# Optimization experiments

Hardware: AMD Instinct MI355X
Metric: run time of the kernel (lower is better)

The kernel has to match this reference:

```python
import jax, jax.numpy as jnp
import numpy as np


def segment_pool(labels, hidden):
    """Faithful vectorized version of get_entity_embedding_from_hidden_states.

    labels: [B, L] int (0=O, 1=B, 2=I); hidden: [B, L, H].
    Returns [B, L, H]: per-row, the first count_ones(row) slots hold the mean
    hidden state of each mention segment (segments delimited by label==1 over
    the nonzero-label token stream, flattened across the whole batch), rest 0.
    """
    B, L, H = hidden.shape
    N = B * L
    lab = labels.reshape(N)
    h = hidden.reshape(N, H)
    m = lab != 0
    # stable sort: nonzero-label tokens first, original order preserved
    perm = jnp.argsort(jnp.logical_not(m))
    lab_s = lab[perm]
    h_s = h[perm]
    m_s = m[perm]
    b = (lab_s == 1).astype(jnp.int32)
    cum = jnp.cumsum(b)                      # ones seen so far (nonzero stream)
    idx0 = jnp.argmax(b)                     # position of first B-tag (0 if none)
    p = jnp.arange(N)
    # chunk id of nonzero-stream token p: (#ones at positions <= p+idx0) - 1
    seg = cum[jnp.minimum(p + idx0, N - 1)] - 1
    valid = m_s & (seg >= 0)
    seg_ids = jnp.where(valid, seg, N)       # invalid tokens -> dumped segment N
    sums = jax.ops.segment_sum(h_s, seg_ids, num_segments=N + 1)[:N]
    counts = jax.ops.segment_sum(valid.astype(h.dtype), seg_ids, num_segments=N + 1)[:N]
    means = sums / jnp.maximum(counts, 1.0)[:, None]   # [N, H]
    # re-split per row: row b consumes count_ones(b) consecutive means, padded to L
    c = jnp.sum(labels == 1, axis=1)         # [B]
    starts = jnp.cumsum(c) - c               # exclusive prefix sum
    j = jnp.arange(L)
    gidx = jnp.clip(starts[:, None] + j[None, :], 0, N - 1)  # [B, L]
    out = means[gidx]                        # [B, L, H]
    return jnp.where((j[None, :] < c[:, None])[:, :, None], out, jnp.zeros((), hidden.dtype))


def setup_inputs() -> dict:
    key = jax.random.key(0)
    ks = jax.random.split(key, 8)
    B, L, H, E, P = 64, 512, 768, 1000, 300
    return {
        "bio_slot_labels": jax.random.randint(ks[0], (B, L), 0, 3, dtype=jnp.int32),
        "hidden_states": jax.random.normal(ks[1], (B, L, H), dtype=jnp.float32),
        "entity_type_embeddings": jax.random.normal(ks[2], (E, H), dtype=jnp.float32),
        "w1": jax.random.normal(ks[3], (H, H), dtype=jnp.float32) * 0.02,
        "b1": jnp.zeros((H,), dtype=jnp.float32),
        "w2": jax.random.normal(ks[4], (H, 3), dtype=jnp.float32) * 0.02,
        "b2": jnp.zeros((3,), dtype=jnp.float32),
        "w_mention": jax.random.normal(ks[5], (H, P), dtype=jnp.float32) * 0.02,
        "w_desc": jax.random.normal(ks[6], (H, P), dtype=jnp.float32) * 0.02,
    }


def reference(bio_slot_labels, hidden_states, entity_type_embeddings,
              w1, b1, w2, b2, w_mention, w_desc):
    # bio_mlp: Linear -> ReLU -> Linear -> LogSoftmax
    h1 = jax.nn.relu(jnp.einsum('blh,hk->blk', hidden_states, w1) + b1)
    bio_slot_logits = jax.nn.log_softmax(jnp.einsum('blh,hc->blc', h1, w2) + b2, axis=-1)
    predicted_bio_slot = jnp.argmax(bio_slot_logits, axis=-1)

    proj_desc = entity_type_embeddings @ w_desc          # [E, 300]

    def score(labels):
        pooled = segment_pool(labels, hidden_states)     # [B, L, H]
        proj_mention = jnp.einsum('blh,hp->blp', pooled, w_mention)
        dot = jnp.einsum('blp,ep->ble', proj_mention, proj_desc)
        return jax.nn.log_softmax(dot, axis=-1)

    return (bio_slot_logits, score(bio_slot_labels), score(predicted_bio_slot))
```

## Files before the change

### kernel.cpp

```cpp
#include <hip/hip_runtime.h>
#include <stdint.h>

__device__ inline float bf2f(unsigned short u) { return __uint_as_float(((unsigned int)u) << 16); }
__device__ inline unsigned short f2bf(float f) {
    unsigned int x = __float_as_uint(f);
    unsigned int r = x + 0x7fffu + ((x >> 16) & 1u);
    return (unsigned short)(r >> 16);
}

typedef __attribute__((ext_vector_type(8))) short bf16x8;
typedef __attribute__((ext_vector_type(4))) float f32x4;
typedef __attribute__((ext_vector_type(4))) int   v4i;
typedef __attribute__((ext_vector_type(4))) unsigned short u16x4;

#define FLAG_CAP 8192
#define MARGIN 0.02

__device__ inline void gload16(const void* g, void* l) {
    __builtin_amdgcn_global_load_lds(
        (const __attribute__((address_space(1))) void*)g,
        (__attribute__((address_space(3))) void*)l, 16, 0, 0);
}

__global__ __launch_bounds__(256) void gemm_bt(
    const unsigned short* __restrict__ A,
    const unsigned short* __restrict__ Bt,
    void* __restrict__ C,
    const int* __restrict__ Mdev,
    const int* __restrict__ rowMap,
    const float* __restrict__ fb1,
    const float* __restrict__ fw2,
    float* __restrict__ fpart,
    int M, int N, int K, int lda, int ldb, int ldc, int mode, int rowOff,
    size_t zA, int zMeta, int zMap, size_t zC)
{
    int zz = blockIdx.z;
    A += (size_t)zz * zA;
    if (Mdev) M = Mdev[zz * zMeta];
    if (rowMap) rowMap += (size_t)zz * zMap;

    int NT = gridDim.x;
    int p  = blockIdx.x + NT * blockIdx.y;
    int i8 = p >> 3;
    int mt = (p & 7) + 8 * (i8 / NT);
    int nt = i8 % NT;

    if (rowOff + mt * 128 >= M) return;

    __shared__ __align__(16) unsigned short As[128 * 64];
    __shared__ __align__(16) unsigned short Bs[128 * 64];

    int tid  = threadIdx.x;
    int lane = tid & 63, wave = tid >> 6;
    int wRow = (wave >> 1) * 64, wCol = (wave & 1) * 64;
    int mBase = mt * 128, nBase = nt * 128;
    int lm = lane & 15, kg = lane >> 4;
    int sr = tid >> 3;
    int sc = (tid & 7) * 8;

    f32x4 acc[4][4] = {};

    for (int k0 = 0; k0 < K; k0 += 64) {
        __syncthreads();
#pragma unroll
        for (int i = 0; i < 4; ++i) {
            int r = sr + 32 * i;
            int gm = rowOff + mBase + r; if (gm > M - 1) gm = M - 1;
            gload16(&A[(size_t)(gm - rowOff) * lda + k0 + sc], &As[wave * 512 + i * 2048]);
            int gn = nBase + r; if (gn > N - 1) gn = N - 1;
            gload16(&Bt[(size_t)gn * ldb + k0 + sc], &Bs[wave * 512 + i * 2048]);
        }
        __syncthreads();
#pragma unroll
        for (int ks = 0; ks < 2; ++ks) {
            bf16x8 af[4], bfr[4];
#pragma unroll
            for (int i = 0; i < 4; ++i) {
                af[i]  = *(const bf16x8*)&As[(wRow + i * 16 + lm) * 64 + ks * 32 + kg * 8];
                bfr[i] = *(const bf16x8*)&Bs[(wCol + i * 16 + lm) * 64 + ks * 32 + kg * 8];
            }
#pragma unroll
            for (int mi = 0; mi < 4; ++mi)
#pragma unroll
                for (int ni = 0; ni < 4; ++ni)
                    acc[mi][ni] = __builtin_amdgcn_mfma_f32_16x16x32_bf16(
                        af[mi], bfr[ni], acc[mi][ni], 0, 0, 0);
        }
    }

    int rbase = (lane >> 4) * 4;

    if (mode == 3) {
        float b1v[4], w2l[4][3];
#pragma unroll
        for (int ni = 0; ni < 4; ++ni) {
            int n = nBase + wCol + ni * 16 + lm;
            b1v[ni] = fb1[n];
#pragma unroll
            for (int c = 0; c < 3; ++c) w2l[ni][c] = fw2[n * 3 + c];
        }
#pragma unroll
        for (int mi = 0; mi < 4; ++mi) {
            float p2[4][3] = {};
#pragma unroll
            for (int ni = 0; ni < 4; ++ni)
#pragma unroll
                for (int r = 0; r < 4; ++r) {
                    float v = acc[mi][ni][r] + b1v[ni];
                    v = fmaxf(v, 0.f);
                    p2[r][0] += v * w2l[ni][0];
                    p2[r][1] += v * w2l[ni][1];
                    p2[r][2] += v * w2l[ni][2];
                }
#pragma unroll
            for (int r = 0; r < 4; ++r)
#pragma unroll
                for (int c = 0; c < 3; ++c) {
                    float s = p2[r][c];
                    s += __shfl_down(s, 8); s += __shfl_down(s, 4);
                    s += __shfl_down(s, 2); s += __shfl_down(s, 1);
                    p2[r][c] = s;
                }
            if (lm == 0) {
#pragma unroll
                for (int r = 0; r < 4; ++r) {
                    int row = mBase + wRow + mi * 16 + rbase + r;
#pragma unroll
                    for (int c = 0; c < 3; ++c)
                        atomicAdd(&fpart[(size_t)row * 3 + c], p2[r][c]);
                }
            }
        }
        return;
    }

#pragma unroll
    for (int mi = 0; mi < 4; ++mi) {
#pragma unroll
        for (int r = 0; r < 4; ++r) {
            int m = rowOff + mBase + wRow + mi * 16 + rbase + r;
            if (m >= M) continue;
            size_t crow = rowMap ? (size_t)rowMap[m] * ldc : (size_t)(m - rowOff) * ldc;
#pragma unroll
            for (int ni = 0; ni < 4; ++ni) {
                int n = nBase + wCol + ni * 16 + lm;
                if (n >= N) continue;
                float v = acc[mi][ni][r];
                if (mode == 2) ((float*)C)[(size_t)zz * zC + crow + n] = v;
                else           ((unsigned short*)C)[crow + n] = f2bf(v);
            }
        }
    }
}

__global__ __launch_bounds__(256) void prep_all(
    const float* __restrict__ ent, unsigned short* __restrict__ entB,
    const float* __restrict__ hidden, unsigned short* __restrict__ hiddenB,
    const float* __restrict__ wd, unsigned short* __restrict__ wdT,
    const float* __restrict__ w1, unsigned short* __restrict__ w1T,
    const float* __restrict__ wm, unsigned short* __restrict__ wmP,
    v4i* __restrict__ zreg)
{
    __shared__ float tile[32][33];
    int b = blockIdx.x, t = threadIdx.x;
    if (b < 373) {
        int i = b * 256 + t;
        if (i < 95312) { v4i z = {0, 0, 0, 0}; zreg[i] = z; }
        return;
    }
    b -= 373;
    if (b < 750) {
        int i = b * 256 + t;
        float4 v = ((const float4*)ent)[i];
        u16x4 o = { f2bf(v.x), f2bf(v.y), f2bf(v.z), f2bf(v.w) };
        ((u16x4*)entB)[i] = o;
        return;
    }
    b -= 750;
    if (b < 24576) {
        int i = b * 256 + t;
        float4 v = ((const float4*)hidden)[i];
        u16x4 o = { f2bf(v.x), f2bf(v.y), f2bf(v.z), f2bf(v.w) };
        ((u16x4*)hiddenB)[i] = o;
        return;
    }
    b -= 24576;
    if (b < 240 + 576) {
        const float* in; unsigned short* out; int R, C, bx, by;
        if (b < 240) { in = wd; out = wdT; R = 768; C = 300; bx = b % 10; by = b / 10; }
        else { int bb = b - 240; in = w1; out = w1T; R = 768; C = 768; bx = bb % 24; by = bb / 24; }
        int tx = t & 31, ty = t >> 5;
        int c0 = bx * 32, r0 = by * 32;
#pragma unroll
        for (int i = 0; i < 4; ++i) {
            int r = r0 + ty + i * 8, c = c0 + tx;
            if (r < R && c < C) tile[ty + i * 8][tx] = in[(size_t)r * C + c];
        }
        __syncthreads();
#pragma unroll
        for (int i = 0; i < 4; ++i) {
            int orow = c0 + ty + i * 8, ocol = r0 + tx;
            if (orow < C && ocol < R) out[(size_t)orow * R + ocol] = f2bf(tile[tx][ty + i * 8]);
        }
        return;
    }
    b -= 816;
    {
        int idx = b * 256 + t;
        if (idx < 768 * 300) wmP[(size_t)(idx / 300) * 320 + (idx % 300)] = f2bf(wm[idx]);
    }
}

__global__ void bio_final2(const float* __restrict__ part, const float* __restrict__ b2,
                           float* __restrict__ out0, int* __restrict__ predLab,
                           int* __restrict__ flagCnt, int* __restrict__ flagList)
{
    int t = blockIdx.x * 256 + threadIdx.x;
    double a[3];
#pragma unroll
    for (int c = 0; c < 3; ++c) a[c] = (double)part[(size_t)t * 3 + c] + (double)b2[c];
    double mx = a[0]; if (a[1] > mx) mx = a[1]; if (a[2] > mx) mx = a[2];
    double ls = mx + log(exp(a[0] - mx) + exp(a[1] - mx) + exp(a[2] - mx));
    out0[t * 3 + 0] = (float)(a[0] - ls);
    out0[t * 3 + 1] = (float)(a[1] - ls);
    out0[t * 3 + 2] = (float)(a[2] - ls);
    int pbest = 0; double bv = a[0];
    if (a[1] > bv) { bv = a[1]; pbest = 1; }
    if (a[2] > bv) { bv = a[2]; pbest = 2; }
    predLab[t] = pbest;
    double second = -1e300;
#pragma unroll
    for (int c = 0; c < 3; ++c) if (c != pbest && a[c] > second) second = a[c];
    if (bv - second < MARGIN) {
        int i = atomicAdd(flagCnt, 1);
        if (i < FLAG_CAP) flagList[i] = t;
    }
}

__global__ __launch_bounds__(256) void h1_bio_gemm(
    const float* __restrict__ hidden, const int* __restrict__ flagList,
    const float* __restrict__ W,
    const float* __restrict__ b1, const float* __restrict__ w2,
    float* __restrict__ part, const int* __restrict__ Mdev, int partStride)
{
    int M = *Mdev; if (M > FLAG_CAP) M = FLAG_CAP;
    if (M <= 0) return;
    int m0 = blockIdx.x * 64, n0 = blockIdx.y * 64;
    if (m0 >= M) return;
    __shared__ float AsT[16][64];
    __shared__ float Ws[16][64];
    int tx = threadIdx.x, ty = threadIdx.y;
    int tid = ty * 16 + tx;
    float acc[4][4] = {};

    for (int k0 = 0; k0 < 768; k0 += 16) {
        __syncthreads();
        {
            int row = tid >> 2, seg = (tid & 3) * 4;
            int gm = m0 + row; if (gm > M - 1) gm = M - 1;
            float4 v = *(const float4*)&hidden[(size_t)flagList[gm] * 768 + k0 + seg];
            AsT[seg + 0][row] = v.x; AsT[seg + 1][row] = v.y;
            AsT[seg + 2][row] = v.z; AsT[seg + 3][row] = v.w;
        }
        {
            int row = tid >> 4, seg = (tid & 15) * 4;
            *(float4*)&Ws[row][seg] = *(const float4*)&W[(size_t)(k0 + row) * 768 + n0 + seg];
        }
        __syncthreads();
#pragma unroll
        for (int kk = 0; kk < 16; ++kk) {
            float4 av = *(const float4*)&AsT[kk][ty * 4];
            float4 bv = *(const float4*)&Ws[kk][tx * 4];
            float a[4] = {av.x, av.y, av.z, av.w};
            float b[4] = {bv.x, bv.y, bv.z, bv.w};
#pragma unroll
            for (int i = 0; i < 4; ++i)
#pragma unroll
                for (int j = 0; j < 4; ++j)
                    acc[i][j] += a[i] * b[j];
        }
    }

    float b1v[4], w2l[4][3];
#pragma unroll
    for (int j = 0; j < 4; ++j) {
        int n = n0 + tx * 4 + j;
        b1v[j] = b1[n];
#pragma unroll
        for (int c = 0; c < 3; ++c) w2l[j][c] = w2[n * 3 + c];
    }
    float p[4][3] = {};
#pragma unroll
    for (int i = 0; i < 4; ++i)
#pragma unroll
        for (int j = 0; j < 4; ++j) {
            float v = acc[i][j] + b1v[j];
            v = fmaxf(v, 0.f);
#pragma unroll
            for (int c = 0; c < 3; ++c) p[i][c] += v * w2l[j][c];
        }
#pragma unroll
    for (int i = 0; i < 4; ++i)
#pragma unroll
        for (int c = 0; c < 3; ++c) {
            float s = p[i][c];
            s += __shfl_down(s, 8); s += __shfl_down(s, 4);
            s += __shfl_down(s, 2); s += __shfl_down(s, 1);
            p[i][c] = s;
        }
    if (tx == 0) {
#pragma unroll
        for (int i = 0; i < 4; ++i) {
            int t = m0 + ty * 4 + i;
            if (t >= M) continue;
#pragma unroll
            for (int c = 0; c < 3; ++c)
                part[(size_t)blockIdx.y * partStride + (size_t)t * 3 + c] = p[i][c];
        }
    }
}

__global__ __launch_bounds__(1024) void seg_prep2(
    const int* __restrict__ labels, int* predLab,
    int* __restrict__ streamTok, int* __restrict__ cumArr,
    int* __restrict__ meta, int* __restrict__ rowC, int* __restrict__ mapArr,
    int* __restrict__ segFirst,
    const float* __restrict__ partF, const float* __restrict__ b2,
    const int* __restrict__ flagList, const int* __restrict__ flagCnt, int partStride)
{
    int setz = blockIdx.x;
    int t = threadIdx.x;

    if (setz == 1) {
        int cnt = *flagCnt; if (cnt > FLAG_CAP) cnt = FLAG_CAP;
        for (int i = t; i < cnt; i += 1024) {
            double a[3] = {(double)b2[0], (double)b2[1], (double)b2[2]};
#pragma unroll
            for (int blk = 0; blk < 12; ++blk)
#pragma unroll
                for (int c = 0; c < 3; ++c)
                    a[c] += (double)partF[(size_t)blk * partStride + (size_t)i * 3 + c];
            int pbest = 0; double bv = a[0];
            if (a[1] > bv) { bv = a[1]; pbest = 1; }
            if (a[2] > bv) { bv = a[2]; pbest = 2; }
            predLab[flagList[i]] = pbest;
        }
        __syncthreads();
    }

    const int* lab = setz ? predLab : labels;
    int* sTok = streamTok + setz * 32768;
    int* sCum = cumArr + setz * 32768;
    int* mt   = meta + setz * 64;
    int* rC   = rowC + setz * 64;
    int* mp   = mapArr + setz * 32768;
    int* sf   = segFirst + setz * 32768;

    __shared__ int sM[1024], sB[1024];
    __shared__ int sRowC[64], sRowStart[64];
    __shared__ int sIdx0;
    if (t == 0) sIdx0 = 0x7fffffff;
    int base = t * 32;
    int vals[32];
#pragma unroll
    for (int j = 0; j < 8; ++j) {
        v4i v = ((const v4i*)lab)[t * 8 + j];
        vals[4 * j + 0] = v[0]; vals[4 * j + 1] = v[1];
        vals[4 * j + 2] = v[2]; vals[4 * j + 3] = v[3];
    }
    int mc = 0, bc = 0;
#pragma unroll
    for (int i = 0; i < 32; ++i) { mc += (vals[i] != 0); bc += (vals[i] == 1); }
    sM[t] = mc; sB[t] = bc; __syncthreads();
    for (int off = 1; off < 1024; off <<= 1) {
        int vm = 0, vb = 0;
        if (t >= off) { vm = sM[t - off]; vb = sB[t - off]; }
        __syncthreads();
        sM[t] += vm; sB[t] += vb;
        __syncthreads();
    }
    int mBase = sM[t] - mc, bBase = sB[t] - bc;
    int mRun = 0, bRun = 0;
#pragma unroll
    for (int i = 0; i < 32; ++i) {
        int v = vals[i];
        if (v != 0) {
            int q = mBase + mRun;
            sTok[q] = base + i;
            int isB = (v == 1);
            sCum[q] = bBase + bRun + isB;
            if (isB && (bBase + bRun) == 0) sIdx0 = q;
            mRun += 1; bRun += isB;
        }
    }
    if ((t & 15) == 0) sRowStart[t >> 4] = bBase;
    __syncthreads();
    if ((t & 15) == 0) {
        int b = t >> 4;
        sRowC[b] = sB[t + 15] - sRowStart[b];
        rC[b] = sRowC[b];
    }
    if (t == 1023) { mt[0] = sB[1023]; mt[1] = sM[1023]; }
    if (t == 0) mt[2] = (sIdx0 == 0x7fffffff) ? 0 : sIdx0;
    __syncthreads();
    for (int idx = t; idx < 32768; idx += 1024) {
        int b = idx >> 9, j = idx & 511;
        if (j < sRowC[b]) mp[sRowStart[b] + j] = idx;
    }

    int K = sM[1023], numB = sB[1023];
    int idx0 = (sIdx0 == 0x7fffffff) ? 0 : sIdx0;
    for (int q = t; q < K; q += 1024) {
        int qq = q + idx0;
        int c  = (qq < K) ? sCum[qq] : numB;
        int sg = c - 1;
        if (sg < 0) continue;
        int sp = -1;
        if (q > 0) {
            int qq2 = qq - 1;
            int c2  = (qq2 < K) ? sCum[qq2] : numB;
            sp = c2 - 1;
        }
        if (sg != sp) sf[sg] = q;
    }
}

__global__ __launch_bounds__(192) void seg_means2(
    const unsigned short* __restrict__ hiddenB, const int* __restrict__ streamTok,
    const int* __restrict__ segFirst, const int* __restrict__ meta,
    unsigned short* __restrict__ means, size_t zMeans)
{
    int setz = blockIdx.y;
    const int* mt = meta + setz * 64;
    int s = blockIdx.x;
    int numB = mt[0];
    if (s >= numB) return;
    const int* st = streamTok + setz * 32768;
    const int* sf = segFirst + setz * 32768;
    int q0 = sf[s];
    int q1 = (s + 1 < numB) ? sf[s + 1] : mt[1];
    int cnt = q1 - q0;
    int t = threadIdx.x;
    float a0 = 0.f, a1 = 0.f, a2 = 0.f, a3 = 0.f;
    for (int i = 0; i < cnt; ++i) {
        const unsigned short* hr = hiddenB + (size_t)st[q0 + i] * 768;
        u16x4 v = *(const u16x4*)&hr[t * 4];
        a0 += bf2f(v[0]); a1 += bf2f(v[1]); a2 += bf2f(v[2]); a3 += bf2f(v[3]);
    }
    float fc = (float)cnt;
    u16x4 o = { f2bf(a0 / fc), f2bf(a1 / fc), f2bf(a2 / fc), f2bf(a3 / fc) };
    *(u16x4*)&means[(size_t)setz * zMeans + (size_t)s * 768 + t * 4] = o;
}

__global__ __launch_bounds__(256) void softmax_rows2(float* __restrict__ outBase,
                                                     const int* __restrict__ rowCBase,
                                                     size_t zC)
{
    float* out = outBase + (size_t)blockIdx.y * zC;
    const int* rowC = rowCBase + blockIdx.y * 64;
    int v = blockIdx.x;
    int b = v >> 9, j = v & 511;
    int t = threadIdx.x;
    float* row = out + (size_t)v * 1000;
    if (j >= rowC[b]) {
        for (int e = t; e < 1000; e += 256) row[e] = -6.907755278982137f;
        return;
    }
    __shared__ float red[256];
    float x0 = row[t];
    float x1 = row[t + 256];
    float x2 = row[t + 512];
    bool has3 = (t + 768) < 1000;
    float x3 = has3 ? row[t + 768] : -1e30f;
    float mx = fmaxf(fmaxf(x0, x1), fmaxf(x2, x3));
    red[t] = mx; __syncthreads();
    for (int st = 128; st > 0; st >>= 1) { if (t < st) red[t] = fmaxf(red[t], red[t + st]); __syncthreads(); }
    float M = red[0]; __syncthreads();
    float sm = expf(x0 - M) + expf(x1 - M) + expf(x2 - M) + (has3 ? expf(x3 - M) : 0.f);
    red[t] = sm; __syncthreads();
    for (int st = 128; st > 0; st >>= 1) { if (t < st) red[t] += red[t + st]; __syncthreads(); }
    float ls = M + logf(red[0]);
    row[t]       = x0 - ls;
    row[t + 256] = x1 - ls;
    row[t + 512] = x2 - ls;
    if (has3) row[t + 768] = x3 - ls;
}

extern "C" void kernel_launch(void* const* d_in, const int* in_sizes, int n_in,
                              void* d_out, int out_size, void* d_ws, size_t ws_size,
                              hipStream_t stream)
{
    (void)in_sizes; (void)n_in; (void)out_size; (void)ws_size;
    const int*   labels = (const int*)d_in[0];
    const float* hidden = (const float*)d_in[1];
    const float* ent    = (const float*)d_in[2];
    const float* w1     = (const float*)d_in[3];
    const float* b1     = (const float*)d_in[4];
    const float* w2     = (const float*)d_in[5];
    const float* b2     = (const float*)d_in[6];
    const float* wm     = (const float*)d_in[7];
    const float* wd     = (const float*)d_in[8];

    char* ws = (char*)d_ws;
    size_t off = 0;
    auto alloc = [&](size_t bytes) {
        void* p = ws + off;
        off = (off + bytes + 255) & ~(size_t)255;
        return p;
    };
    int* meta      = (int*)alloc(512);
    int* rowC      = (int*)alloc(512);
    int* predLab   = (int*)alloc(32768 * 4);
    int* streamTok = (int*)alloc(2 * 32768 * 4);
    int* cumArr    = (int*)alloc(2 * 32768 * 4);
    int* segFirst  = (int*)alloc(2 * 32768 * 4);
    int* mapArr    = (int*)alloc(2 * 32768 * 4);
    int* flagList  = (int*)alloc(FLAG_CAP * 4);
    unsigned short* entB = (unsigned short*)alloc((size_t)1000 * 768 * 2);
    unsigned short* wdT  = (unsigned short*)alloc((size_t)300 * 768 * 2);
    unsigned short* W2t  = (unsigned short*)alloc((size_t)1000 * 768 * 2);
    unsigned short* w1T  = (unsigned short*)alloc((size_t)768 * 768 * 2);
    unsigned short* hiddenB = (unsigned short*)alloc((size_t)32768 * 768 * 2);
    float* partF = (float*)alloc((size_t)12 * FLAG_CAP * 3 * 4);
    char* zbase = (char*)alloc(1524992);
    unsigned short* pd  = (unsigned short*)zbase;
    unsigned short* wmP = (unsigned short*)(zbase + 640000);
    float* part         = (float*)(zbase + 1131520);
    int* flagCnt        = (int*)(zbase + 1524736);
    unsigned short* means = (unsigned short*)alloc((size_t)2 * 32768 * 768 * 2);

    float* out0 = (float*)d_out;
    float* out1 = out0 + 98304;

    prep_all<<<27415, 256, 0, stream>>>(ent, entB, hidden, hiddenB, wd, wdT,
                                        w1, w1T, wm, wmP, (v4i*)zbase);

    gemm_bt<<<dim3(3, 8), 256, 0, stream>>>(entB, wdT, pd, nullptr, nullptr,
                                            nullptr, nullptr, nullptr,
                                            1000, 300, 768, 768, 768, 320, 0, 0,
                                            0, 0, 0, 0);
    gemm_bt<<<dim3(6, 8), 256, 0, stream>>>(pd, wmP, W2t, nullptr, nullptr,
                                            nullptr, nullptr, nullptr,
                                            1000, 768, 320, 320, 320, 768, 0, 0,
                                            0, 0, 0, 0);

    gemm_bt<<<dim3(6, 256), 256, 0, stream>>>(hiddenB, w1T, nullptr, nullptr, nullptr,
                                              b1, w2, part,
                                              32768, 768, 768, 768, 768, 0, 3, 0,
                                              0, 0, 0, 0);
    bio_final2<<<128, 256, 0, stream>>>(part, b2, out0, predLab, flagCnt, flagList);
    h1_bio_gemm<<<dim3(FLAG_CAP / 64, 12), dim3(16, 16), 0, stream>>>(
        hidden, flagList, w1, b1, w2, partF, flagCnt, FLAG_CAP * 3);

    seg_prep2<<<2, 1024, 0, stream>>>(labels, predLab, streamTok, cumArr, meta, rowC,
                                      mapArr, segFirst, partF, b2, flagList, flagCnt,
                                      FLAG_CAP * 3);
    seg_means2<<<dim3(32768, 2), 192, 0, stream>>>(hiddenB, streamTok, segFirst, meta,
                                                   means, (size_t)32768 * 768);
    gemm_bt<<<dim3(8, 256, 2), 256, 0, stream>>>(means, W2t, out1, meta, mapArr,
                                                 nullptr, nullptr, nullptr,
                                                 0, 1000, 768, 768, 768, 1000, 2, 0,
                                                 (size_t)32768 * 768, 64, 32768,
                                                 (size_t)32768 * 1000);
    softmax_rows2<<<dim3(32768, 2), 256, 0, stream>>>(out1, rowC, (size_t)32768 * 1000);
}
```

Baseline: 807.7 us.

## Merge small GEMM launches into combined kernels and vectorize row softmax

The generic GEMM kernel becomes a device function, and the small entity-projection GEMMs are packed into the same launches as the big bio GEMM and the bio-final step. This removes several kernel launches and their tail idle time. The block swizzle now uses a plain mt/nt index, which changes the order tiles run in and may affect cache reuse. The row log-softmax now uses float4 loads and wave shuffle reductions in place of a shared-memory tree, cutting barriers and memory instructions on a large memory-bound pass.

```diff
diff --git a/kernel.cpp b/kernel.cpp
--- a/kernel.cpp
+++ b/kernel.cpp
@@ -22,7 +22,7 @@
         (__attribute__((address_space(3))) void*)l, 16, 0, 0);
 }
 
-__global__ __launch_bounds__(256) void gemm_bt(
+static __device__ inline void dev_gemm(
     const unsigned short* __restrict__ A,
     const unsigned short* __restrict__ Bt,
     void* __restrict__ C,
@@ -31,24 +31,12 @@
     const float* __restrict__ fb1,
     const float* __restrict__ fw2,
     float* __restrict__ fpart,
-    int M, int N, int K, int lda, int ldb, int ldc, int mode, int rowOff,
-    size_t zA, int zMeta, int zMap, size_t zC)
-{
-    int zz = blockIdx.z;
-    A += (size_t)zz * zA;
-    if (Mdev) M = Mdev[zz * zMeta];
-    if (rowMap) rowMap += (size_t)zz * zMap;
-
-    int NT = gridDim.x;
-    int p  = blockIdx.x + NT * blockIdx.y;
-    int i8 = p >> 3;
-    int mt = (p & 7) + 8 * (i8 / NT);
-    int nt = i8 % NT;
-
-    if (rowOff + mt * 128 >= M) return;
-
-    __shared__ __align__(16) unsigned short As[128 * 64];
-    __shared__ __align__(16) unsigned short Bs[128 * 64];
+    int M, int N, int K, int lda, int ldb, int ldc, int mode,
+    int mt, int nt,
+    unsigned short* As, unsigned short* Bs)
+{
+    if (Mdev) M = *Mdev;
+    if (mt * 128 >= M) return;
 
     int tid  = threadIdx.x;
     int lane = tid & 63, wave = tid >> 6;
@@ -65,8 +53,8 @@
 #pragma unroll
         for (int i = 0; i < 4; ++i) {
             int r = sr + 32 * i;
-            int gm = rowOff + mBase + r; if (gm > M - 1) gm = M - 1;
-            gload16(&A[(size_t)(gm - rowOff) * lda + k0 + sc], &As[wave * 512 + i * 2048]);
+            int gm = mBase + r; if (gm > M - 1) gm = M - 1;
+            gload16(&A[(size_t)gm * lda + k0 + sc], &As[wave * 512 + i * 2048]);
             int gn = nBase + r; if (gn > N - 1) gn = N - 1;
             gload16(&Bt[(size_t)gn * ldb + k0 + sc], &Bs[wave * 512 + i * 2048]);
         }
@@ -138,84 +126,26 @@
     for (int mi = 0; mi < 4; ++mi) {
 #pragma unroll
         for (int r = 0; r < 4; ++r) {
-            int m = rowOff + mBase + wRow + mi * 16 + rbase + r;
+            int m = mBase + wRow + mi * 16 + rbase + r;
             if (m >= M) continue;
-            size_t crow = rowMap ? (size_t)rowMap[m] * ldc : (size_t)(m - rowOff) * ldc;
+            size_t crow = rowMap ? (size_t)rowMap[m] * ldc : (size_t)m * ldc;
 #pragma unroll
             for (int ni = 0; ni < 4; ++ni) {
                 int n = nBase + wCol + ni * 16 + lm;
                 if (n >= N) continue;
                 float v = acc[mi][ni][r];
-                if (mode == 2) ((float*)C)[(size_t)zz * zC + crow + n] = v;
+                if (mode == 2) ((float*)C)[crow + n] = v;
                 else           ((unsigned short*)C)[crow + n] = f2bf(v);
             }
         }
     }
 }
 
-__global__ __launch_bounds__(256) void prep_all(
-    const float* __restrict__ ent, unsigned short* __restrict__ entB,
-    const float* __restrict__ hidden, unsigned short* __restrict__ hiddenB,
-    const float* __restrict__ wd, unsigned short* __restrict__ wdT,
-    const float* __restrict__ w1, unsigned short* __restrict__ w1T,
-    const float* __restrict__ wm, unsigned short* __restrict__ wmP,
-    v4i* __restrict__ zreg)
-{
-    __shared__ float tile[32][33];
-    int b = blockIdx.x, t = threadIdx.x;
-    if (b < 373) {
-        int i = b * 256 + t;
-        if (i < 95312) { v4i z = {0, 0, 0, 0}; zreg[i] = z; }
-        return;
-    }
-    b -= 373;
-    if (b < 750) {
-        int i = b * 256 + t;
-        float4 v = ((const float4*)ent)[i];
-        u16x4 o = { f2bf(v.x), f2bf(v.y), f2bf(v.z), f2bf(v.w) };
-        ((u16x4*)entB)[i] = o;
-        return;
-    }
-    b -= 750;
-    if (b < 24576) {
-        int i = b * 256 + t;
-        float4 v = ((const float4*)hidden)[i];
-        u16x4 o = { f2bf(v.x), f2bf(v.y), f2bf(v.z), f2bf(v.w) };
-        ((u16x4*)hiddenB)[i] = o;
-        return;
-    }
-    b -= 24576;
-    if (b < 240 + 576) {
-        const float* in; unsigned short* out; int R, C, bx, by;
-        if (b < 240) { in = wd; out = wdT; R = 768; C = 300; bx = b % 10; by = b / 10; }
-        else { int bb = b - 240; in = w1; out = w1T; R = 768; C = 768; bx = bb % 24; by = bb / 24; }
-        int tx = t & 31, ty = t >> 5;
-        int c0 = bx * 32, r0 = by * 32;
-#pragma unroll
-        for (int i = 0; i < 4; ++i) {
-            int r = r0 + ty + i * 8, c = c0 + tx;
-            if (r < R && c < C) tile[ty + i * 8][tx] = in[(size_t)r * C + c];
-        }
-        __syncthreads();
-#pragma unroll
-        for (int i = 0; i < 4; ++i) {
-            int orow = c0 + ty + i * 8, ocol = r0 + tx;
-            if (orow < C && ocol < R) out[(size_t)orow * R + ocol] = f2bf(tile[tx][ty + i * 8]);
-        }
-        return;
-    }
-    b -= 816;
-    {
-        int idx = b * 256 + t;
-        if (idx < 768 * 300) wmP[(size_t)(idx / 300) * 320 + (idx % 300)] = f2bf(wm[idx]);
-    }
-}
-
-__global__ void bio_final2(const float* __restrict__ part, const float* __restrict__ b2,
-                           float* __restrict__ out0, int* __restrict__ predLab,
-                           int* __restrict__ flagCnt, int* __restrict__ flagList)
-{
-    int t = blockIdx.x * 256 + threadIdx.x;
+static __device__ inline void dev_final2(int t, const float* __restrict__ part,
+                                         const float* __restrict__ b2,
+                                         float* __restrict__ out0, int* __restrict__ predLab,
+                                         int* __restrict__ flagCnt, int* __restrict__ flagList)
+{
     double a[3];
 #pragma unroll
     for (int c = 0; c < 3; ++c) a[c] = (double)part[(size_t)t * 3 + c] + (double)b2[c];
@@ -237,6 +167,116 @@
     }
 }
 
+__global__ __launch_bounds__(256) void k_gemms1(
+    const unsigned short* __restrict__ hiddenB, const unsigned short* __restrict__ w1T,
+    const float* __restrict__ b1, const float* __restrict__ w2, float* __restrict__ part,
+    const unsigned short* __restrict__ entB, const unsigned short* __restrict__ wdT,
+    unsigned short* __restrict__ pd)
+{
+    __shared__ __align__(16) unsigned short As[128 * 64];
+    __shared__ __align__(16) unsigned short Bs[128 * 64];
+    int bx = blockIdx.x;
+    if (bx < 1536) {
+        dev_gemm(hiddenB, w1T, nullptr, nullptr, nullptr, b1, w2, part,
+                 32768, 768, 768, 768, 768, 0, 3, bx / 6, bx % 6, As, Bs);
+    } else {
+        bx -= 1536;
+        dev_gemm(entB, wdT, pd, nullptr, nullptr, nullptr, nullptr, nullptr,
+                 1000, 300, 768, 768, 768, 320, 0, bx / 3, bx % 3, As, Bs);
+    }
+}
+
+__global__ __launch_bounds__(256) void k_gemms2(
+    const unsigned short* __restrict__ pd, const unsigned short* __restrict__ wmP,
+    unsigned short* __restrict__ W2t,
+    const float* __restrict__ part, const float* __restrict__ b2,
+    float* __restrict__ out0, int* __restrict__ predLab,
+    int* __restrict__ flagCnt, int* __restrict__ flagList)
+{
+    __shared__ __align__(16) unsigned short As[128 * 64];
+    __shared__ __align__(16) unsigned short Bs[128 * 64];
+    int bx = blockIdx.x;
+    if (bx < 48) {
+        dev_gemm(pd, wmP, W2t, nullptr, nullptr, nullptr, nullptr, nullptr,
+                 1000, 768, 320, 320, 320, 768, 0, bx / 6, bx % 6, As, Bs);
+    } else {
+        dev_final2((bx - 48) * 256 + threadIdx.x, part, b2, out0, predLab,
+                   flagCnt, flagList);
+    }
+}
+
+__global__ __launch_bounds__(256) void gemm_score(
+    const unsigned short* __restrict__ means, const unsigned short* __restrict__ W2t,
+    float* __restrict__ out1, const int* __restrict__ meta, const int* __restrict__ mapArr)
+{
+    __shared__ __align__(16) unsigned short As[128 * 64];
+    __shared__ __align__(16) unsigned short Bs[128 * 64];
+    int zz = blockIdx.z;
+    dev_gemm(means + (size_t)zz * 32768 * 768, W2t,
+             out1 + (size_t)zz * 32768 * 1000,
+             meta + zz * 64, mapArr + zz * 32768,
+             nullptr, nullptr, nullptr,
+             0, 1000, 768, 768, 768, 1000, 2, blockIdx.y, blockIdx.x, As, Bs);
+}
+
+__global__ __launch_bounds__(256) void prep_all(
+    const float* __restrict__ ent, unsigned short* __restrict__ entB,
+    const float* __restrict__ hidden, unsigned short* __restrict__ hiddenB,
+    const float* __restrict__ wd, unsigned short* __restrict__ wdT,
+    const float* __restrict__ w1, unsigned short* __restrict__ w1T,
+    const float* __restrict__ wm, unsigned short* __restrict__ wmP,
+    v4i* __restrict__ zreg)
+{
+    __shared__ float tile[32][33];
+    int b = blockIdx.x, t = threadIdx.x;
+    if (b < 373) {
+        int i = b * 256 + t;
+        if (i < 95312) { v4i z = {0, 0, 0, 0}; zreg[i] = z; }
+        return;
+    }
+    b -= 373;
+    if (b < 750) {
+        int i = b * 256 + t;
+        float4 v = ((const float4*)ent)[i];
+        u16x4 o = { f2bf(v.x), f2bf(v.y), f2bf(v.z), f2bf(v.w) };
+        ((u16x4*)entB)[i] = o;
+        return;
+    }
+    b -= 750;
+    if (b < 24576) {
+        int i = b * 256 + t;
+        float4 v = ((const float4*)hidden)[i];
+        u16x4 o = { f2bf(v.x), f2bf(v.y), f2bf(v.z), f2bf(v.w) };
+        ((u16x4*)hiddenB)[i] = o;
+        return;
+    }
+    b -= 24576;
+    if (b < 240 + 576) {
+        const float* in; unsigned short* out; int R, C, bx, by;
+        if (b < 240) { in = wd; out = wdT; R = 768; C = 300; bx = b % 10; by = b / 10; }
+        else { int bb = b - 240; in = w1; out = w1T; R = 768; C = 768; bx = bb % 24; by = bb / 24; }
+        int tx = t & 31, ty = t >> 5;
+        int c0 = bx * 32, r0 = by * 32;
+#pragma unroll
+        for (int i = 0; i < 4; ++i) {
+            int r = r0 + ty + i * 8, c = c0 + tx;
+            if (r < R && c < C) tile[ty + i * 8][tx] = in[(size_t)r * C + c];
+        }
+        __syncthreads();
+#pragma unroll
+        for (int i = 0; i < 4; ++i) {
+            int orow = c0 + ty + i * 8, ocol = r0 + tx;
+            if (orow < C && ocol < R) out[(size_t)orow * R + ocol] = f2bf(tile[tx][ty + i * 8]);
+        }
+        return;
+    }
+    b -= 816;
+    {
+        int idx = b * 256 + t;
+        if (idx < 768 * 300) wmP[(size_t)(idx / 300) * 320 + (idx % 300)] = f2bf(wm[idx]);
+    }
+}
+
 __global__ __launch_bounds__(256) void h1_bio_gemm(
     const float* __restrict__ hidden, const int* __restrict__ flagList,
     const float* __restrict__ W,
@@ -249,8 +289,8 @@
     if (m0 >= M) return;
     __shared__ float AsT[16][64];
     __shared__ float Ws[16][64];
-    int tx = threadIdx.x, ty = threadIdx.y;
-    int tid = ty * 16 + tx;
+    int tx = threadIdx.x & 15, ty = threadIdx.x >> 4;
+    int tid = threadIdx.x;
     float acc[4][4] = {};
 
     for (int k0 = 0; k0 < 768; k0 += 16) {
@@ -462,28 +502,35 @@
     int b = v >> 9, j = v & 511;
     int t = threadIdx.x;
     float* row = out + (size_t)v * 1000;
+    bool act = t < 250;
     if (j >= rowC[b]) {
-        for (int e = t; e < 1000; e += 256) row[e] = -6.907755278982137f;
+        if (act) {
+            float4 f; f.x = f.y = f.z = f.w = -6.907755278982137f;
+            ((float4*)row)[t] = f;
+        }
         return;
     }
-    __shared__ float red[256];
-    float x0 = row[t];
-    float x1 = row[t + 256];
-    float x2 = row[t + 512];
-    bool has3 = (t + 768) < 1000;
-    float x3 = has3 ? row[t + 768] : -1e30f;
-    float mx = fmaxf(fmaxf(x0, x1), fmaxf(x2, x3));
-    red[t] = mx; __syncthreads();
-    for (int st = 128; st > 0; st >>= 1) { if (t < st) red[t] = fmaxf(red[t], red[t + st]); __syncthreads(); }
-    float M = red[0]; __syncthreads();
-    float sm = expf(x0 - M) + expf(x1 - M) + expf(x2 - M) + (has3 ? expf(x3 - M) : 0.f);
-    red[t] = sm; __syncthreads();
-    for (int st = 128; st > 0; st >>= 1) { if (t < st) red[t] += red[t + st]; __syncthreads(); }
-    float ls = M + logf(red[0]);
-    row[t]       = x0 - ls;
-    row[t + 256] = x1 - ls;
-    row[t + 512] = x2 - ls;
-    if (has3) row[t + 768] = x3 - ls;
+    __shared__ float wr[4], ws[4];
+    int wave = t >> 6, lane = t & 63;
+    float4 x;
+    if (act) x = ((const float4*)row)[t];
+    else { x.x = x.y = x.z = x.w = -1e30f; }
+    float mx = fmaxf(fmaxf(x.x, x.y), fmaxf(x.z, x.w));
+#pragma unroll
+    for (int o = 32; o > 0; o >>= 1) mx = fmaxf(mx, __shfl_xor(mx, o));
+    if (lane == 0) wr[wave] = mx;
+    __syncthreads();
+    float M = fmaxf(fmaxf(wr[0], wr[1]), fmaxf(wr[2], wr[3]));
+    float sm = act ? (expf(x.x - M) + expf(x.y - M) + expf(x.z - M) + expf(x.w - M)) : 0.f;
+#pragma unroll
+    for (int o = 32; o > 0; o >>= 1) sm += __shfl_xor(sm, o);
+    if (lane == 0) ws[wave] = sm;
+    __syncthreads();
+    float ls = M + logf(ws[0] + ws[1] + ws[2] + ws[3]);
+    if (act) {
+        x.x -= ls; x.y -= ls; x.z -= ls; x.w -= ls;
+        ((float4*)row)[t] = x;
+    }
 }
 
 extern "C" void kernel_launch(void* const* d_in, const int* in_sizes, int n_in,
@@ -534,33 +581,17 @@
 
     prep_all<<<27415, 256, 0, stream>>>(ent, entB, hidden, hiddenB, wd, wdT,
                                         w1, w1T, wm, wmP, (v4i*)zbase);
-
-    gemm_bt<<<dim3(3, 8), 256, 0, stream>>>(entB, wdT, pd, nullptr, nullptr,
-                                            nullptr, nullptr, nullptr,
-                                            1000, 300, 768, 768, 768, 320, 0, 0,
-                                            0, 0, 0, 0);
-    gemm_bt<<<dim3(6, 8), 256, 0, stream>>>(pd, wmP, W2t, nullptr, nullptr,
-                                            nullptr, nullptr, nullptr,
-                                            1000, 768, 320, 320, 320, 768, 0, 0,
-                                            0, 0, 0, 0);
-
-    gemm_bt<<<dim3(6, 256), 256, 0, stream>>>(hiddenB, w1T, nullptr, nullptr, nullptr,
-                                              b1, w2, part,
-                                              32768, 768, 768, 768, 768, 0, 3, 0,
-                                              0, 0, 0, 0);
-    bio_final2<<<128, 256, 0, stream>>>(part, b2, out0, predLab, flagCnt, flagList);
-    h1_bio_gemm<<<dim3(FLAG_CAP / 64, 12), dim3(16, 16), 0, stream>>>(
+    k_gemms1<<<1536 + 24, 256, 0, stream>>>(hiddenB, w1T, b1, w2, part,
+                                            entB, wdT, pd);
+    k_gemms2<<<48 + 128, 256, 0, stream>>>(pd, wmP, W2t,
+                                           part, b2, out0, predLab, flagCnt, flagList);
+    h1_bio_gemm<<<dim3(FLAG_CAP / 64, 12), 256, 0, stream>>>(
         hidden, flagList, w1, b1, w2, partF, flagCnt, FLAG_CAP * 3);
-
     seg_prep2<<<2, 1024, 0, stream>>>(labels, predLab, streamTok, cumArr, meta, rowC,
                                       mapArr, segFirst, partF, b2, flagList, flagCnt,
                                       FLAG_CAP * 3);
     seg_means2<<<dim3(32768, 2), 192, 0, stream>>>(hiddenB, streamTok, segFirst, meta,
                                                    means, (size_t)32768 * 768);
-    gemm_bt<<<dim3(8, 256, 2), 256, 0, stream>>>(means, W2t, out1, meta, mapArr,
-                                                 nullptr, nullptr, nullptr,
-                                                 0, 1000, 768, 768, 768, 1000, 2, 0,
-                                                 (size_t)32768 * 768, 64, 32768,
-                                                 (size_t)32768 * 1000);
+    gemm_score<<<dim3(8, 256, 2), 256, 0, stream>>>(means, W2t, out1, meta, mapArr);
     softmax_rows2<<<dim3(32768, 2), 256, 0, stream>>>(out1, rowC, (size_t)32768 * 1000);
 }
```

New measurement: 909.5 us. 12.6% more time.

## Double-buffer GEMM LDS tiles and use wave-shuffle float4 log-softmax

Applied to the files above, without the earlier changes.

The GEMM main loop now stages 32-wide K slices into two LDS buffers, prefetching the next slice while MFMAs run on the current one. This replaces the single 64-wide buffer that needed two barriers per step. The grouped tile swizzle is dropped in favour of a plain blockIdx mapping, which may reduce L2 reuse. The row log-softmax uses float4 loads and stores with wavefront shuffle reductions instead of an LDS tree reduction with many barriers.

```diff
diff --git a/kernel.cpp b/kernel.cpp
--- a/kernel.cpp
+++ b/kernel.cpp
@@ -39,53 +39,52 @@
     if (Mdev) M = Mdev[zz * zMeta];
     if (rowMap) rowMap += (size_t)zz * zMap;
 
-    int NT = gridDim.x;
-    int p  = blockIdx.x + NT * blockIdx.y;
-    int i8 = p >> 3;
-    int mt = (p & 7) + 8 * (i8 / NT);
-    int nt = i8 % NT;
-
+    int nt = blockIdx.x, mt = blockIdx.y;
     if (rowOff + mt * 128 >= M) return;
 
-    __shared__ __align__(16) unsigned short As[128 * 64];
-    __shared__ __align__(16) unsigned short Bs[128 * 64];
+    __shared__ __align__(16) unsigned short As[2][128 * 32];
+    __shared__ __align__(16) unsigned short Bs[2][128 * 32];
 
     int tid  = threadIdx.x;
     int lane = tid & 63, wave = tid >> 6;
     int wRow = (wave >> 1) * 64, wCol = (wave & 1) * 64;
     int mBase = mt * 128, nBase = nt * 128;
     int lm = lane & 15, kg = lane >> 4;
-    int sr = tid >> 3;
-    int sc = (tid & 7) * 8;
+    int sr = tid >> 2;
+    int sc = (tid & 3) * 8;
+
+    auto STAGE = [&](int k0, int buf) {
+#pragma unroll
+        for (int i = 0; i < 2; ++i) {
+            int r = sr + 64 * i;
+            int gm = rowOff + mBase + r; if (gm > M - 1) gm = M - 1;
+            gload16(&A[(size_t)(gm - rowOff) * lda + k0 + sc], &As[buf][wave * 512 + i * 2048]);
+            int gn = nBase + r; if (gn > N - 1) gn = N - 1;
+            gload16(&Bt[(size_t)gn * ldb + k0 + sc], &Bs[buf][wave * 512 + i * 2048]);
+        }
+    };
 
     f32x4 acc[4][4] = {};
 
-    for (int k0 = 0; k0 < K; k0 += 64) {
-        __syncthreads();
+    STAGE(0, 0);
+    __syncthreads();
+    int nsteps = K >> 5;
+    for (int s = 0; s < nsteps; ++s) {
+        int cur = s & 1;
+        if (s + 1 < nsteps) STAGE((s + 1) << 5, cur ^ 1);
+        bf16x8 af[4], bfr[4];
 #pragma unroll
         for (int i = 0; i < 4; ++i) {
-            int r = sr + 32 * i;
-            int gm = rowOff + mBase + r; if (gm > M - 1) gm = M - 1;
-            gload16(&A[(size_t)(gm - rowOff) * lda + k0 + sc], &As[wave * 512 + i * 2048]);
-            int gn = nBase + r; if (gn > N - 1) gn = N - 1;
-            gload16(&Bt[(size_t)gn * ldb + k0 + sc], &Bs[wave * 512 + i * 2048]);
-        }
-        __syncthreads();
-#pragma unroll
-        for (int ks = 0; ks < 2; ++ks) {
-            bf16x8 af[4], bfr[4];
-#pragma unroll
-            for (int i = 0; i < 4; ++i) {
-                af[i]  = *(const bf16x8*)&As[(wRow + i * 16 + lm) * 64 + ks * 32 + kg * 8];
-                bfr[i] = *(const bf16x8*)&Bs[(wCol + i * 16 + lm) * 64 + ks * 32 + kg * 8];
-            }
-#pragma unroll
-            for (int mi = 0; mi < 4; ++mi)
-#pragma unroll
-                for (int ni = 0; ni < 4; ++ni)
-                    acc[mi][ni] = __builtin_amdgcn_mfma_f32_16x16x32_bf16(
-                        af[mi], bfr[ni], acc[mi][ni], 0, 0, 0);
-        }
+            af[i]  = *(const bf16x8*)&As[cur][(wRow + i * 16 + lm) * 32 + kg * 8];
+            bfr[i] = *(const bf16x8*)&Bs[cur][(wCol + i * 16 + lm) * 32 + kg * 8];
+        }
+#pragma unroll
+        for (int mi = 0; mi < 4; ++mi)
+#pragma unroll
+            for (int ni = 0; ni < 4; ++ni)
+                acc[mi][ni] = __builtin_amdgcn_mfma_f32_16x16x32_bf16(
+                    af[mi], bfr[ni], acc[mi][ni], 0, 0, 0);
+        __syncthreads();
     }
 
     int rbase = (lane >> 4) * 4;
@@ -462,28 +461,35 @@
     int b = v >> 9, j = v & 511;
     int t = threadIdx.x;
     float* row = out + (size_t)v * 1000;
+    bool act = t < 250;
     if (j >= rowC[b]) {
-        for (int e = t; e < 1000; e += 256) row[e] = -6.907755278982137f;
+        if (act) {
+            float4 f; f.x = f.y = f.z = f.w = -6.907755278982137f;
+            ((float4*)row)[t] = f;
+        }
         return;
     }
-    __shared__ float red[256];
-    float x0 = row[t];
-    float x1 = row[t + 256];
-    float x2 = row[t + 512];
-    bool has3 = (t + 768) < 1000;
-    float x3 = has3 ? row[t + 768] : -1e30f;
-    float mx = fmaxf(fmaxf(x0, x1), fmaxf(x2, x3));
-    red[t] = mx; __syncthreads();
-    for (int st = 128; st > 0; st >>= 1) { if (t < st) red[t] = fmaxf(red[t], red[t + st]); __syncthreads(); }
-    float M = red[0]; __syncthreads();
-    float sm = expf(x0 - M) + expf(x1 - M) + expf(x2 - M) + (has3 ? expf(x3 - M) : 0.f);
-    red[t] = sm; __syncthreads();
-    for (int st = 128; st > 0; st >>= 1) { if (t < st) red[t] += red[t + st]; __syncthreads(); }
-    float ls = M + logf(red[0]);
-    row[t]       = x0 - ls;
-    row[t + 256] = x1 - ls;
-    row[t + 512] = x2 - ls;
-    if (has3) row[t + 768] = x3 - ls;
+    __shared__ float wr[4], ws[4];
+    int wave = t >> 6, lane = t & 63;
+    float4 x;
+    if (act) x = ((const float4*)row)[t];
+    else { x.x = x.y = x.z = x.w = -1e30f; }
+    float mx = fmaxf(fmaxf(x.x, x.y), fmaxf(x.z, x.w));
+#pragma unroll
+    for (int o = 32; o > 0; o >>= 1) mx = fmaxf(mx, __shfl_xor(mx, o));
+    if (lane == 0) wr[wave] = mx;
+    __syncthreads();
+    float M = fmaxf(fmaxf(wr[0], wr[1]), fmaxf(wr[2], wr[3]));
+    float sm = act ? (expf(x.x - M) + expf(x.y - M) + expf(x.z - M) + expf(x.w - M)) : 0.f;
+#pragma unroll
+    for (int o = 32; o > 0; o >>= 1) sm += __shfl_xor(sm, o);
+    if (lane == 0) ws[wave] = sm;
+    __syncthreads();
+    float ls = M + logf(ws[0] + ws[1] + ws[2] + ws[3]);
+    if (act) {
+        x.x -= ls; x.y -= ls; x.z -= ls; x.w -= ls;
+        ((float4*)row)[t] = x;
+    }
 }
 
 extern "C" void kernel_launch(void* const* d_in, const int* in_sizes, int n_in,
```

After: 781.9 us. -3.2%, faster.
